# Performance work log

Hardware: AMD Instinct MI355X
Metric: run time of the kernel (lower is better)

The kernel has to match this reference:

```python
import jax, jax.numpy as jnp
import numpy as np
from jax import lax

B = 2          # graphs per batch
N_PER = 8192   # points per graph
K = 64         # max_num_neighbors in radius()
RATIO1, R1 = 0.5, 0.2
RATIO2, R2 = 0.25, 0.4


def _init(key, shape):
    return 0.1 * jax.random.normal(key, shape, jnp.float32)


def setup_inputs() -> dict:
    key = jax.random.key(0)
    ks = jax.random.split(key, 16)
    inp = {}
    inp["pos"] = jax.random.uniform(ks[0], (B * N_PER, 3), jnp.float32)
    inp["batch"] = jnp.repeat(jnp.arange(B, dtype=jnp.int32), N_PER)
    i = 1
    for name, dims in [("sa1", [(3, 64), (64, 64), (64, 128)]),
                       ("sa2", [(131, 128), (128, 128), (128, 256)])]:
        for j, (a, b) in enumerate(dims, 1):
            inp[f"{name}_W{j}"] = _init(ks[i], (a, b)); i += 1
            inp[f"{name}_b{j}"] = jnp.zeros((b,), jnp.float32)
    for name, (a, b) in [("lin1", (256, 256)), ("lin2", (256, 128)), ("lin3", (128, 1))]:
        inp[f"{name}_W"] = _init(ks[i], (a, b)); i += 1
        inp[f"{name}_b"] = jnp.zeros((b,), jnp.float32)
    return inp


def _fps(pts, S):
    # farthest point sampling; pts [n,3] -> idx [S] (deterministic start at 0)
    n = pts.shape[0]
    d0 = jnp.full((n,), jnp.inf, pts.dtype)
    def body(carry, _):
        d, last = carry
        d = jnp.minimum(d, jnp.sum((pts - pts[last]) ** 2, axis=-1))
        nxt = jnp.argmax(d).astype(jnp.int32)
        return (d, nxt), last
    _, idx = lax.scan(body, (d0, jnp.int32(0)), None, length=S)
    return idx


def _mlp(h, Ws, bs):
    h = jax.nn.relu(h @ Ws[0] + bs[0])
    h = jax.nn.relu(h @ Ws[1] + bs[1])
    return h @ Ws[2] + bs[2]


def _sa(x, pos, ratio, r, Ws, bs):
    # PointNet++ set abstraction: FPS -> radius neighbors (<=K) -> edge MLP -> max
    # pos [B,n,3]; x [B,n,C] or None
    n = pos.shape[1]
    S = int(n * ratio)
    idx = jax.vmap(lambda p: _fps(p, S))(pos)                       # [B,S]
    q = jnp.take_along_axis(pos, idx[..., None], axis=1)             # [B,S,3]
    d2 = jnp.sum((q[:, :, None, :] - pos[:, None, :, :]) ** 2, -1)   # [B,S,n]
    d2 = jnp.where(d2 <= r * r, d2, jnp.inf)
    negd, nbr = lax.top_k(-d2, K)                                    # [B,S,K]
    valid = jnp.isfinite(negd)                                       # in-radius mask
    gat = jax.vmap(lambda a, i: a[i])                                # per-graph gather
    rel = gat(pos, nbr) - q[:, :, None, :]                           # [B,S,K,3]
    feat = rel if x is None else jnp.concatenate([gat(x, nbr), rel], axis=-1)
    h = _mlp(feat, Ws, bs)                                           # [B,S,K,C]
    h = jnp.where(valid[..., None], h, -jnp.inf)
    return jnp.max(h, axis=2), q                                     # scatter-max aggr


def reference(pos, batch,
              sa1_W1, sa1_b1, sa1_W2, sa1_b2, sa1_W3, sa1_b3,
              sa2_W1, sa2_b1, sa2_W2, sa2_b2, sa2_W3, sa2_b3,
              lin1_W, lin1_b, lin2_W, lin2_b, lin3_W, lin3_b):
    p = pos.reshape(B, N_PER, 3)  # batch ids are sorted, equal-sized graphs
    x1, p1 = _sa(None, p, RATIO1, R1,
                 (sa1_W1, sa1_W2, sa1_W3), (sa1_b1, sa1_b2, sa1_b3))
    x2, _ = _sa(x1, p1, RATIO2, R2,
                (sa2_W1, sa2_W2, sa2_W3), (sa2_b1, sa2_b2, sa2_b3))
    h = jax.nn.relu(x2 @ lin1_W + lin1_b)
    h = jax.nn.relu(h @ lin2_W + lin2_b)
    h = jax.nn.sigmoid(h @ lin3_W + lin3_b)
    return h.reshape(-1, 1)  # [B * N_PER * RATIO1 * RATIO2, 1]
```

## Files before the change

### kernel.cpp

```cpp
#include <hip/hip_runtime.h>
#include <math.h>

#define NEG_INF (-__builtin_inff())
#define POS_INF (__builtin_inff())

__device__ __forceinline__ int imax_i(int a, int b) { return a > b ? a : b; }

template<int CTRL, int RMASK>
__device__ __forceinline__ int dpp_imax_step(int y) {
  const int t = __builtin_amdgcn_update_dpp(y, y, CTRL, RMASK, 0xf, false);
  return imax_i(y, t);
}

template<int N, int PPT, int S, int NT>
__global__ __launch_bounds__(NT) void fpsp_kernel(const float* __restrict__ pos,
                                                  float* __restrict__ q_out)
{
  constexpr int CELLS = 4096;
  constexpr int CPT = CELLS / NT;
  static_assert(N == NT * PPT, "chunking");
  static_assert(S <= CELLS, "winner list fits in hist");

  const int b = blockIdx.x;
  const int t = threadIdx.x;
  pos += (size_t)b * N * 3;
  q_out += (size_t)b * S * 3;

  __shared__ float sxyz[3 * N];
  __shared__ int sorder[N];
  __shared__ int hist[CELLS];
  __shared__ int scanbuf[NT];
  __shared__ unsigned long long slot[4];

  int* const swin = hist;

  for (int i = t; i < CELLS; i += NT) hist[i] = 0;
  if (t < 4) slot[t] = 0;
  __syncthreads();
  for (int i = t; i < N; i += NT) {
    const float x = pos[3*i+0], y = pos[3*i+1], z = pos[3*i+2];
    sxyz[3*i+0] = x; sxyz[3*i+1] = y; sxyz[3*i+2] = z;
    int cx = (int)(x * 16.f); cx = cx < 0 ? 0 : (cx > 15 ? 15 : cx);
    int cy = (int)(y * 16.f); cy = cy < 0 ? 0 : (cy > 15 ? 15 : cy);
    int cz = (int)(z * 16.f); cz = cz < 0 ? 0 : (cz > 15 ? 15 : cz);
    int m = 0;
#pragma unroll
    for (int k = 0; k < 4; ++k)
      m |= (((cx >> k) & 1) << (3*k+2)) | (((cy >> k) & 1) << (3*k+1)) | (((cz >> k) & 1) << (3*k));
    atomicAdd(&hist[m], 1);
  }
  __syncthreads();
  int loc[CPT]; int run = 0;
#pragma unroll
  for (int j = 0; j < CPT; ++j) { loc[j] = run; run += hist[t*CPT + j]; }
  scanbuf[t] = run;
  __syncthreads();
  for (int off = 1; off < NT; off <<= 1) {
    const int o = (t >= off) ? scanbuf[t - off] : 0;
    __syncthreads();
    scanbuf[t] += o;
    __syncthreads();
  }
  const int base = scanbuf[t] - run;
#pragma unroll
  for (int j = 0; j < CPT; ++j) hist[t*CPT + j] = base + loc[j];
  __syncthreads();
  for (int i = t; i < N; i += NT) {
    const float x = sxyz[3*i+0], y = sxyz[3*i+1], z = sxyz[3*i+2];
    int cx = (int)(x * 16.f); cx = cx < 0 ? 0 : (cx > 15 ? 15 : cx);
    int cy = (int)(y * 16.f); cy = cy < 0 ? 0 : (cy > 15 ? 15 : cy);
    int cz = (int)(z * 16.f); cz = cz < 0 ? 0 : (cz > 15 ? 15 : cz);
    int m = 0;
#pragma unroll
    for (int k = 0; k < 4; ++k)
      m |= (((cx >> k) & 1) << (3*k+2)) | (((cy >> k) & 1) << (3*k+1)) | (((cz >> k) & 1) << (3*k));
    const int sl = atomicAdd(&hist[m], 1);
    sorder[sl] = i;
  }
  __syncthreads();
  float px[PPT], py[PPT], pz[PPT], d[PPT];
  int og[PPT];
  float bxmin = POS_INF, bxmax = NEG_INF, bymin = POS_INF, bymax = NEG_INF,
        bzmin = POS_INF, bzmax = NEG_INF;
#pragma unroll
  for (int j = 0; j < PPT; ++j) {
    const int o = sorder[t*PPT + j];
    og[j] = o;
    const float x = sxyz[3*o+0], y = sxyz[3*o+1], z = sxyz[3*o+2];
    px[j] = x; py[j] = y; pz[j] = z;
    bxmin = fminf(bxmin, x); bxmax = fmaxf(bxmax, x);
    bymin = fminf(bymin, y); bymax = fmaxf(bymax, y);
    bzmin = fminf(bzmin, z); bzmax = fmaxf(bzmax, z);
    d[j] = POS_INF;
  }
  __syncthreads();

  const int lane = t & 63;
  float cval = POS_INF;
  int corig = 0x7fffffff;
  int wmvb = 0;
  int wwo = 0x7fffffff;
  int worig = 0;
  int p = 0;

  for (int it = 0; it < S; ++it) {
    if (t == 0) swin[it] = worig;
    const float lx = sxyz[3*worig+0], ly = sxyz[3*worig+1], lz = sxyz[3*worig+2];

    const float ddx = fmaxf(0.f, fmaxf(bxmin - lx, lx - bxmax));
    const float ddy = fmaxf(0.f, fmaxf(bymin - ly, ly - bymax));
    const float ddz = fmaxf(0.f, fmaxf(bzmin - lz, lz - bzmax));
    const float mind2 = ddx*ddx + ddy*ddy + ddz*ddz;
    const bool rec = !(mind2 * 0.99999f >= cval);

    if (rec) {
      float bv = -1.f; int bo = 0x7fffffff;
#pragma unroll
      for (int j = 0; j < PPT; ++j) {
        const float dx = __fsub_rn(px[j], lx);
        const float dy = __fsub_rn(py[j], ly);
        const float dz = __fsub_rn(pz[j], lz);
        const float nd = __fadd_rn(__fadd_rn(__fmul_rn(dx, dx), __fmul_rn(dy, dy)),
                                   __fmul_rn(dz, dz));
        const float dn = __builtin_fminf(d[j], nd);
        d[j] = dn;
        if (dn > bv || (dn == bv && og[j] < bo)) { bv = dn; bo = og[j]; }
      }
      cval = bv; corig = bo;
    }

    if (__ballot(rec) != 0ULL) {
      const int x = __float_as_int(cval);
      int y = x;
      y = dpp_imax_step<0x111, 0xf>(y);
      y = dpp_imax_step<0x112, 0xf>(y);
      y = dpp_imax_step<0x114, 0xf>(y);
      y = dpp_imax_step<0x118, 0xf>(y);
      y = dpp_imax_step<0x142, 0xa>(y);
      y = dpp_imax_step<0x143, 0xc>(y);
      wmvb = __builtin_amdgcn_readlane(y, 63);
      unsigned long long tie = __ballot(__float_as_int(cval) == wmvb);
      int wo = 0x7fffffff;
      while (tie) {
        const int l = __builtin_ctzll(tie);
        const int o = __builtin_amdgcn_readlane(corig, l);
        wo = wo < o ? wo : o;
        tie &= tie - 1;
      }
      wwo = wo;
    }

    if (lane == 0)
      atomicMax(&slot[p], ((unsigned long long)(unsigned)wmvb << 32) |
                          (unsigned)~(unsigned)wwo);
    if (t == 0) slot[(p + 1) & 3] = 0;
    __syncthreads();
    const unsigned long long wm = slot[p];
    worig = (int)(~(unsigned)(wm & 0xffffffffULL));
    p = (p + 1) & 3;
  }

  __syncthreads();
  for (int s = t; s < S; s += NT) {
    const int o = swin[s];
    q_out[3*s+0] = sxyz[3*o+0]; q_out[3*s+1] = sxyz[3*o+1]; q_out[3*s+2] = sxyz[3*o+2];
  }
}

struct Prod2S {
  unsigned long long slot[4];
  float sxyz[3 * 4096];
  int sorder[4096];
  int hist[4096];
  int scanbuf[1024];
};
struct Cons1S {
  unsigned long long keys[2048];
  float sW2[64 * 64];
  float sW3[64 * 128];
  float sW1[3 * 64];
  float sb1[64], sb2[64], sb3[128];
  float h1[64][65];
  float h2b[64][65];
  float featT[3][64];
  int snb[64];
  int s_cnt;
};
constexpr size_t SMC = sizeof(Prod2S) > sizeof(Cons1S) ? sizeof(Prod2S) : sizeof(Cons1S);

__global__ __launch_bounds__(1024)
void combo2_kernel(const float* __restrict__ pos,
                   const float* __restrict__ q1,
                   float* __restrict__ q2,
                   float* __restrict__ x1,
                   const float* __restrict__ W1, const float* __restrict__ b1,
                   const float* __restrict__ W2, const float* __restrict__ b2,
                   const float* __restrict__ W3, const float* __restrict__ b3)
{
  __shared__ __align__(16) char smraw[SMC];
  const int bid = blockIdx.x;
  const int t = threadIdx.x;

  if (bid < 2) {
    constexpr int N = 4096, PPT = 4, S = 1024, NT = 1024;
    constexpr int CELLS = 4096, CPT = CELLS / NT;
    Prod2S& P = *reinterpret_cast<Prod2S*>(smraw);
    const float* pb = q1 + (size_t)bid * N * 3;
    float* qb = q2 + (size_t)bid * S * 3;
    int* const swin = P.hist;

    for (int i = t; i < CELLS; i += NT) P.hist[i] = 0;
    if (t < 4) P.slot[t] = 0;
    __syncthreads();
    for (int i = t; i < N; i += NT) {
      const float x = pb[3*i+0], y = pb[3*i+1], z = pb[3*i+2];
      P.sxyz[3*i+0] = x; P.sxyz[3*i+1] = y; P.sxyz[3*i+2] = z;
      int cx = (int)(x * 16.f); cx = cx < 0 ? 0 : (cx > 15 ? 15 : cx);
      int cy = (int)(y * 16.f); cy = cy < 0 ? 0 : (cy > 15 ? 15 : cy);
      int cz = (int)(z * 16.f); cz = cz < 0 ? 0 : (cz > 15 ? 15 : cz);
      int m = 0;
#pragma unroll
      for (int k = 0; k < 4; ++k)
        m |= (((cx >> k) & 1) << (3*k+2)) | (((cy >> k) & 1) << (3*k+1)) | (((cz >> k) & 1) << (3*k));
      atomicAdd(&P.hist[m], 1);
    }
    __syncthreads();
    int loc[CPT]; int run = 0;
#pragma unroll
    for (int j = 0; j < CPT; ++j) { loc[j] = run; run += P.hist[t*CPT + j]; }
    P.scanbuf[t] = run;
    __syncthreads();
    for (int off = 1; off < NT; off <<= 1) {
      const int o = (t >= off) ? P.scanbuf[t - off] : 0;
      __syncthreads();
      P.scanbuf[t] += o;
      __syncthreads();
    }
    const int base = P.scanbuf[t] - run;
#pragma unroll
    for (int j = 0; j < CPT; ++j) P.hist[t*CPT + j] = base + loc[j];
    __syncthreads();
    for (int i = t; i < N; i += NT) {
      const float x = P.sxyz[3*i+0], y = P.sxyz[3*i+1], z = P.sxyz[3*i+2];
      int cx = (int)(x * 16.f); cx = cx < 0 ? 0 : (cx > 15 ? 15 : cx);
      int cy = (int)(y * 16.f); cy = cy < 0 ? 0 : (cy > 15 ? 15 : cy);
      int cz = (int)(z * 16.f); cz = cz < 0 ? 0 : (cz > 15 ? 15 : cz);
      int m = 0;
#pragma unroll
      for (int k = 0; k < 4; ++k)
        m |= (((cx >> k) & 1) << (3*k+2)) | (((cy >> k) & 1) << (3*k+1)) | (((cz >> k) & 1) << (3*k));
      const int sl = atomicAdd(&P.hist[m], 1);
      P.sorder[sl] = i;
    }
    __syncthreads();
    float px[PPT], py[PPT], pz[PPT], d[PPT];
    int og[PPT];
    float bxmin = POS_INF, bxmax = NEG_INF, bymin = POS_INF, bymax = NEG_INF,
          bzmin = POS_INF, bzmax = NEG_INF;
#pragma unroll
    for (int j = 0; j < PPT; ++j) {
      const int o = P.sorder[t*PPT + j];
      og[j] = o;
      const float x = P.sxyz[3*o+0], y = P.sxyz[3*o+1], z = P.sxyz[3*o+2];
      px[j] = x; py[j] = y; pz[j] = z;
      bxmin = fminf(bxmin, x); bxmax = fmaxf(bxmax, x);
      bymin = fminf(bymin, y); bymax = fmaxf(bymax, y);
      bzmin = fminf(bzmin, z); bzmax = fmaxf(bzmax, z);
      d[j] = POS_INF;
    }
    __syncthreads();

    const int lane = t & 63;
    float cval = POS_INF;
    int corig = 0x7fffffff;
    int wmvb = 0;
    int wwo = 0x7fffffff;
    int worig = 0;
    int p = 0;

    for (int it = 0; it < S; ++it) {
      if (t == 0) swin[it] = worig;
      const float lx = P.sxyz[3*worig+0], ly = P.sxyz[3*worig+1], lz = P.sxyz[3*worig+2];

      const float ddx = fmaxf(0.f, fmaxf(bxmin - lx, lx - bxmax));
      const float ddy = fmaxf(0.f, fmaxf(bymin - ly, ly - bymax));
      const float ddz = fmaxf(0.f, fmaxf(bzmin - lz, lz - bzmax));
      const float mind2 = ddx*ddx + ddy*ddy + ddz*ddz;
      const bool rec = !(mind2 * 0.99999f >= cval);

      if (rec) {
        float bv = -1.f; int bo = 0x7fffffff;
#pragma unroll
        for (int j = 0; j < PPT; ++j) {
          const float dx = __fsub_rn(px[j], lx);
          const float dy = __fsub_rn(py[j], ly);
          const float dz = __fsub_rn(pz[j], lz);
          const float nd = __fadd_rn(__fadd_rn(__fmul_rn(dx, dx), __fmul_rn(dy, dy)),
                                     __fmul_rn(dz, dz));
          const float dn = __builtin_fminf(d[j], nd);
          d[j] = dn;
          if (dn > bv || (dn == bv && og[j] < bo)) { bv = dn; bo = og[j]; }
        }
        cval = bv; corig = bo;
      }

      if (__ballot(rec) != 0ULL) {
        const int x = __float_as_int(cval);
        int y = x;
        y = dpp_imax_step<0x111, 0xf>(y);
        y = dpp_imax_step<0x112, 0xf>(y);
        y = dpp_imax_step<0x114, 0xf>(y);
        y = dpp_imax_step<0x118, 0xf>(y);
        y = dpp_imax_step<0x142, 0xa>(y);
        y = dpp_imax_step<0x143, 0xc>(y);
        wmvb = __builtin_amdgcn_readlane(y, 63);
        unsigned long long tie = __ballot(__float_as_int(cval) == wmvb);
        int wo = 0x7fffffff;
        while (tie) {
          const int l = __builtin_ctzll(tie);
          const int o = __builtin_amdgcn_readlane(corig, l);
          wo = wo < o ? wo : o;
          tie &= tie - 1;
        }
        wwo = wo;
      }

      if (lane == 0)
        atomicMax(&P.slot[p], ((unsigned long long)(unsigned)wmvb << 32) |
                              (unsigned)~(unsigned)wwo);
      if (t == 0) P.slot[(p + 1) & 3] = 0;
      __syncthreads();
      const unsigned long long wm = P.slot[p];
      worig = (int)(~(unsigned)(wm & 0xffffffffULL));
      p = (p + 1) & 3;
    }

    __syncthreads();
    for (int s = t; s < S; s += NT) {
      const int o = swin[s];
      qb[3*s+0] = P.sxyz[3*o+0]; qb[3*s+1] = P.sxyz[3*o+1]; qb[3*s+2] = P.sxyz[3*o+2];
    }
    return;
  }

  Cons1S& C = *reinterpret_cast<Cons1S*>(smraw);
  const float R1SQ = (float)(0.2 * 0.2);
  const int qi = bid - 2;
  const int g = qi >> 12;
  const float* cb = pos + (size_t)g * 8192 * 3;
  const float qx = q1[3*qi+0], qy = q1[3*qi+1], qz = q1[3*qi+2];

  for (int i = t; i < 192; i += 1024) C.sW1[i] = W1[i];
  if (t < 64) { C.sb1[t] = b1[t]; C.sb2[t] = b2[t]; }
  for (int i = t; i < 4096; i += 1024) C.sW2[i] = W2[i];
  for (int i = t; i < 8192; i += 1024) C.sW3[i] = W3[i];
  if (t < 128) C.sb3[t] = b3[t];
  if (t == 0) C.s_cnt = 0;
  __syncthreads();

  for (int i = t; i < 8192; i += 1024) {
    const float dx = __fsub_rn(cb[3*i+0], qx);
    const float dy = __fsub_rn(cb[3*i+1], qy);
    const float dz = __fsub_rn(cb[3*i+2], qz);
    const float d2 = __fadd_rn(__fadd_rn(__fmul_rn(dx, dx), __fmul_rn(dy, dy)),
                               __fmul_rn(dz, dz));
    if (d2 <= R1SQ) {
      const int pp = atomicAdd(&C.s_cnt, 1);
      if (pp < 2048)
        C.keys[pp] = ((unsigned long long)__float_as_uint(d2) << 32) | (unsigned)i;
    }
  }
  __syncthreads();
  const int M = min(C.s_cnt, 2048);
  const int cnt = min(M, 64);
  if (M > 64) {
    int P2 = 128; while (P2 < M) P2 <<= 1;
    for (int i = M + t; i < P2; i += 1024) C.keys[i] = ~0ULL;
    __syncthreads();
    for (int k = 2; k <= P2; k <<= 1) {
      for (int j = k >> 1; j > 0; j >>= 1) {
        for (int i = t; i < P2; i += 1024) {
          const int l = i ^ j;
          if (l > i) {
            const unsigned long long a = C.keys[i], c = C.keys[l];
            const bool up = ((i & k) == 0);
            if ((a > c) == up) { C.keys[i] = c; C.keys[l] = a; }
          }
        }
        __syncthreads();
      }
    }
  }
  if (t < 64) C.snb[t] = (t < cnt) ? (int)(C.keys[t] & 0xffffffffu) : 0;
  __syncthreads();

  const int e = t & 63, cg = t >> 6;
  if (t < 64) {
    float r0 = 0.f, r1 = 0.f, r2v = 0.f;
    if (t < cnt) {
      const int nb = C.snb[t];
      r0 = cb[3*nb+0] - qx;
      r1 = cb[3*nb+1] - qy;
      r2v = cb[3*nb+2] - qz;
    }
    C.featT[0][t] = r0; C.featT[1][t] = r1; C.featT[2][t] = r2v;
  }
  __syncthreads();
  {
    const int c0 = cg * 4;
    const float a0 = C.featT[0][e], a1 = C.featT[1][e], a2 = C.featT[2][e];
#pragma unroll
    for (int i = 0; i < 4; ++i) {
      float v = C.sb1[c0+i];
      v = fmaf(a0, C.sW1[0*64 + c0+i], v);
      v = fmaf(a1, C.sW1[1*64 + c0+i], v);
      v = fmaf(a2, C.sW1[2*64 + c0+i], v);
      C.h1[e][c0+i] = fmaxf(v, 0.f);
    }
  }
  __syncthreads();
  {
    const int c0 = cg * 4;
    float acc[4];
#pragma unroll
    for (int i = 0; i < 4; ++i) acc[i] = C.sb2[c0+i];
    for (int k = 0; k < 64; ++k) {
      const float a = C.h1[e][k];
      const float4 w = *reinterpret_cast<const float4*>(&C.sW2[k*64 + c0]);
      acc[0] = fmaf(a, w.x, acc[0]);
      acc[1] = fmaf(a, w.y, acc[1]);
      acc[2] = fmaf(a, w.z, acc[2]);
      acc[3] = fmaf(a, w.w, acc[3]);
    }
#pragma unroll
    for (int i = 0; i < 4; ++i) C.h2b[e][c0+i] = fmaxf(acc[i], 0.f);
  }
  __syncthreads();
  float acc3[8];
  const int c0h = cg * 8;
  {
#pragma unroll
    for (int i = 0; i < 8; ++i) acc3[i] = C.sb3[c0h+i];
    for (int k = 0; k < 64; ++k) {
      const float a = C.h2b[e][k];
      const float4* wp = reinterpret_cast<const float4*>(&C.sW3[k*128 + c0h]);
      const float4 w0 = wp[0], w1 = wp[1];
      acc3[0] = fmaf(a, w0.x, acc3[0]);
      acc3[1] = fmaf(a, w0.y, acc3[1]);
      acc3[2] = fmaf(a, w0.z, acc3[2]);
      acc3[3] = fmaf(a, w0.w, acc3[3]);
      acc3[4] = fmaf(a, w1.x, acc3[4]);
      acc3[5] = fmaf(a, w1.y, acc3[5]);
      acc3[6] = fmaf(a, w1.z, acc3[6]);
      acc3[7] = fmaf(a, w1.w, acc3[7]);
    }
  }
  __syncthreads();
  {
    const bool valid = (e < cnt);
#pragma unroll
    for (int i = 0; i < 8; ++i) {
      const float v = valid ? acc3[i] : NEG_INF;
      const int c = c0h + i;
      if (c < 64) C.h1[e][c] = v; else C.h2b[e][c-64] = v;
    }
  }
  __syncthreads();
  if (t < 128) {
    float m = NEG_INF;
    if (t < 64) {
      for (int ee = 0; ee < 64; ++ee) m = fmaxf(m, C.h1[ee][t]);
    } else {
      for (int ee = 0; ee < 64; ++ee) m = fmaxf(m, C.h2b[ee][t-64]);
    }
    x1[(size_t)qi*128 + t] = m;
  }
}

#define KNN_CAP 2048

__global__ __launch_bounds__(256) void knn_kernel(const float* __restrict__ cand,
                                                  const float* __restrict__ qpos,
                                                  int nq_per_graph, int n_cand, float r2,
                                                  int* __restrict__ nbr_out,
                                                  int* __restrict__ cnt_out)
{
  const int qi = blockIdx.x;
  const int t = threadIdx.x;
  const int b = qi / nq_per_graph;
  const float* cb = cand + (size_t)b * n_cand * 3;
  const float qx = qpos[3*qi+0], qy = qpos[3*qi+1], qz = qpos[3*qi+2];

  __shared__ unsigned long long keys[KNN_CAP];
  __shared__ int s_cnt;
  if (t == 0) s_cnt = 0;
  __syncthreads();

  for (int i = t; i < n_cand; i += 256) {
    const float dx = __fsub_rn(cb[3*i+0], qx);
    const float dy = __fsub_rn(cb[3*i+1], qy);
    const float dz = __fsub_rn(cb[3*i+2], qz);
    const float d2 = __fadd_rn(__fadd_rn(__fmul_rn(dx, dx), __fmul_rn(dy, dy)),
                               __fmul_rn(dz, dz));
    if (d2 <= r2) {
      const int p = atomicAdd(&s_cnt, 1);
      if (p < KNN_CAP) keys[p] = ((unsigned long long)__float_as_uint(d2) << 32) | (unsigned)i;
    }
  }
  __syncthreads();
  const int M = min(s_cnt, KNN_CAP);
  const int out_n = min(M, 64);
  if (M > 64) {
    int P = 128; while (P < M) P <<= 1;
    for (int i = M + t; i < P; i += 256) keys[i] = ~0ULL;
    __syncthreads();
    for (int k = 2; k <= P; k <<= 1) {
      for (int j = k >> 1; j > 0; j >>= 1) {
        for (int i = t; i < P; i += 256) {
          const int l = i ^ j;
          if (l > i) {
            const unsigned long long a = keys[i], c = keys[l];
            const bool up = ((i & k) == 0);
            if ((a > c) == up) { keys[i] = c; keys[l] = a; }
          }
        }
        __syncthreads();
      }
    }
  }
  if (t < 64) nbr_out[(size_t)qi*64 + t] = (t < out_n) ? (int)(keys[t] & 0xffffffffu) : -1;
  if (t == 0) cnt_out[qi] = out_n;
}

__global__ __launch_bounds__(256) void mlp2_kernel(const float* __restrict__ q1,
                                                   const float* __restrict__ x1,
                                                   const float* __restrict__ q2,
                                                   const int* __restrict__ nbr,
                                                   const int* __restrict__ cnt_,
                                                   const float* __restrict__ W1, const float* __restrict__ b1,
                                                   const float* __restrict__ W2, const float* __restrict__ b2,
                                                   const float* __restrict__ W3, const float* __restrict__ b3,
                                                   float* __restrict__ x2)
{
  const int qi = blockIdx.x;
  const int t = threadIdx.x;
  const int bg = qi >> 10;
  const float* cb = q1 + (size_t)bg * 4096 * 3;
  const float* xb = x1 + (size_t)bg * 4096 * 128;

  __shared__ float sW[131*128];
  __shared__ float sb[256];
  __shared__ float featT[131][64];
  __shared__ float hbuf[64][129];
  __shared__ int snb[64];

  const int cnt = cnt_[qi];
  const float qx = q2[3*qi+0], qy = q2[3*qi+1], qz = q2[3*qi+2];

  if (t < 64) {
    const int nb = (t < cnt) ? nbr[(size_t)qi*64 + t] : 0;
    snb[t] = nb;
    float r0 = 0.f, r1 = 0.f, r2v = 0.f;
    if (t < cnt) {
      r0 = cb[3*nb+0] - qx;
      r1 = cb[3*nb+1] - qy;
      r2v = cb[3*nb+2] - qz;
    }
    featT[128][t] = r0; featT[129][t] = r1; featT[130][t] = r2v;
  }
  for (int i = t; i < 131*128; i += 256) sW[i] = W1[i];
  if (t < 128) sb[t] = b1[t];
  __syncthreads();
  for (int idx = t; idx < 64*128; idx += 256) {
    const int e = idx >> 7, k = idx & 127;
    featT[k][e] = (e < cnt) ? xb[(size_t)snb[e]*128 + k] : 0.f;
  }
  __syncthreads();

  const int e = t & 63, cg = t >> 6, c0 = cg * 32;
  float acc[32];
  {
#pragma unroll
    for (int i = 0; i < 32; ++i) acc[i] = sb[c0+i];
    for (int k = 0; k < 131; ++k) {
      const float a = featT[k][e];
      const float4* wp = reinterpret_cast<const float4*>(&sW[k*128 + c0]);
#pragma unroll
      for (int i = 0; i < 8; ++i) {
        const float4 w = wp[i];
        acc[4*i+0] = fmaf(a, w.x, acc[4*i+0]);
        acc[4*i+1] = fmaf(a, w.y, acc[4*i+1]);
        acc[4*i+2] = fmaf(a, w.z, acc[4*i+2]);
        acc[4*i+3] = fmaf(a, w.w, acc[4*i+3]);
      }
    }
#pragma unroll
    for (int i = 0; i < 32; ++i) hbuf[e][c0+i] = fmaxf(acc[i], 0.f);
  }
  __syncthreads();
  for (int i = t; i < 128*128; i += 256) sW[i] = W2[i];
  if (t < 128) sb[t] = b2[t];
  __syncthreads();
  {
#pragma unroll
    for (int i = 0; i < 32; ++i) acc[i] = sb[c0+i];
    for (int k = 0; k < 128; ++k) {
      const float a = hbuf[e][k];
      const float4* wp = reinterpret_cast<const float4*>(&sW[k*128 + c0]);
#pragma unroll
      for (int i = 0; i < 8; ++i) {
        const float4 w = wp[i];
        acc[4*i+0] = fmaf(a, w.x, acc[4*i+0]);
        acc[4*i+1] = fmaf(a, w.y, acc[4*i+1]);
        acc[4*i+2] = fmaf(a, w.z, acc[4*i+2]);
        acc[4*i+3] = fmaf(a, w.w, acc[4*i+3]);
      }
    }
  }
  __syncthreads();
#pragma unroll
  for (int i = 0; i < 32; ++i) featT[c0+i][e] = fmaxf(acc[i], 0.f);
  __syncthreads();
  for (int hh = 0; hh < 2; ++hh) {
    for (int i = t; i < 128*128; i += 256) {
      const int k = i >> 7, c = i & 127;
      sW[i] = W3[k*256 + hh*128 + c];
    }
    if (t < 128) sb[t] = b3[hh*128 + t];
    __syncthreads();
#pragma unroll
    for (int i = 0; i < 32; ++i) acc[i] = sb[c0+i];
    for (int k = 0; k < 128; ++k) {
      const float a = featT[k][e];
      const float4* wp = reinterpret_cast<const float4*>(&sW[k*128 + c0]);
#pragma unroll
      for (int i = 0; i < 8; ++i) {
        const float4 w = wp[i];
        acc[4*i+0] = fmaf(a, w.x, acc[4*i+0]);
        acc[4*i+1] = fmaf(a, w.y, acc[4*i+1]);
        acc[4*i+2] = fmaf(a, w.z, acc[4*i+2]);
        acc[4*i+3] = fmaf(a, w.w, acc[4*i+3]);
      }
    }
    const bool valid = (e < cnt);
#pragma unroll
    for (int i = 0; i < 32; ++i) hbuf[e][c0+i] = valid ? acc[i] : NEG_INF;
    __syncthreads();
    if (t < 128) {
      float m = NEG_INF;
      for (int ee = 0; ee < 64; ++ee) m = fmaxf(m, hbuf[ee][t]);
      x2[(size_t)qi*256 + hh*128 + t] = m;
    }
    __syncthreads();
  }
}

__global__ __launch_bounds__(256) void head_kernel(const float* __restrict__ x2,
                                                   const float* __restrict__ W1, const float* __restrict__ b1,
                                                   const float* __restrict__ W2, const float* __restrict__ b2,
                                                   const float* __restrict__ W3, const float* __restrict__ b3,
                                                   float* __restrict__ out)
{
  const int pt = blockIdx.x;
  const int t = threadIdx.x;
  __shared__ float sx[256];
  __shared__ float sh1[256];
  __shared__ float sh2[128];
  __shared__ float red[128];

  sx[t] = x2[(size_t)pt*256 + t];
  __syncthreads();
  float a1 = b1[t];
  for (int k = 0; k < 256; ++k) a1 = fmaf(sx[k], W1[k*256 + t], a1);
  sh1[t] = fmaxf(a1, 0.f);
  __syncthreads();
  if (t < 128) {
    float a2 = b2[t];
    for (int k = 0; k < 256; ++k) a2 = fmaf(sh1[k], W2[k*128 + t], a2);
    sh2[t] = fmaxf(a2, 0.f);
  }
  __syncthreads();
  if (t < 128) red[t] = sh2[t] * W3[t];
  __syncthreads();
  for (int o = 64; o > 0; o >>= 1) {
    if (t < o) red[t] += red[t + o];
    __syncthreads();
  }
  if (t == 0) {
    const float v = red[0] + b3[0];
    out[pt] = 1.f / (1.f + expf(-v));
  }
}

extern "C" void kernel_launch(void* const* d_in, const int* in_sizes, int n_in,
                              void* d_out, int out_size, void* d_ws, size_t ws_size,
                              hipStream_t stream)
{
  (void)in_sizes; (void)n_in; (void)out_size; (void)ws_size;
  const float* pos  = (const float*)d_in[0];
  const float* s1W1 = (const float*)d_in[2];  const float* s1b1 = (const float*)d_in[3];
  const float* s1W2 = (const float*)d_in[4];  const float* s1b2 = (const float*)d_in[5];
  const float* s1W3 = (const float*)d_in[6];  const float* s1b3 = (const float*)d_in[7];
  const float* s2W1 = (const float*)d_in[8];  const float* s2b1 = (const float*)d_in[9];
  const float* s2W2 = (const float*)d_in[10]; const float* s2b2 = (const float*)d_in[11];
  const float* s2W3 = (const float*)d_in[12]; const float* s2b3 = (const float*)d_in[13];
  const float* l1W  = (const float*)d_in[14]; const float* l1b  = (const float*)d_in[15];
  const float* l2W  = (const float*)d_in[16]; const float* l2b  = (const float*)d_in[17];
  const float* l3W  = (const float*)d_in[18]; const float* l3b  = (const float*)d_in[19];
  float* out = (float*)d_out;

  char* w = (char*)d_ws;
  size_t off = 0;
  auto alloc = [&](size_t bytes) -> void* {
    void* p = w + off;
    off += (bytes + 255) & ~(size_t)255;
    return p;
  };
  float* q1   = (float*)alloc((size_t)2*4096*3*4);
  float* q2   = (float*)alloc((size_t)2*1024*3*4);
  float* x1   = (float*)alloc((size_t)8192*128*4);
  float* x2   = (float*)alloc((size_t)2048*256*4);
  int*   nbr2 = (int*)alloc((size_t)2048*64*4);
  int*   cnt2 = (int*)alloc((size_t)2048*4);

  const float R2SQ = (float)(0.4 * 0.4);

  fpsp_kernel<8192, 8, 4096, 1024><<<dim3(2), dim3(1024), 0, stream>>>(pos, q1);
  combo2_kernel<<<dim3(8194), dim3(1024), 0, stream>>>(pos, q1, q2, x1,
                                                       s1W1, s1b1, s1W2, s1b2, s1W3, s1b3);
  knn_kernel<<<dim3(2048), dim3(256), 0, stream>>>(q1, q2, 1024, 4096, R2SQ, nbr2, cnt2);
  mlp2_kernel<<<dim3(2048), dim3(256), 0, stream>>>(q1, x1, q2, nbr2, cnt2,
                                                    s2W1, s2b1, s2W2, s2b2, s2W3, s2b3, x2);
  head_kernel<<<dim3(2048), dim3(256), 0, stream>>>(x2, l1W, l1b, l2W, l2b, l3W, l3b, out);
}
```

Baseline: 4.794 ms.

## Fuse radius kNN, SA2 edge MLP and head MLP into one tail kernel

```diff
diff --git a/kernel.cpp b/kernel.cpp
--- a/kernel.cpp
+++ b/kernel.cpp
@@ -479,101 +479,98 @@
 
 #define KNN_CAP 2048
 
-__global__ __launch_bounds__(256) void knn_kernel(const float* __restrict__ cand,
-                                                  const float* __restrict__ qpos,
-                                                  int nq_per_graph, int n_cand, float r2,
-                                                  int* __restrict__ nbr_out,
-                                                  int* __restrict__ cnt_out)
+struct TailS {
+  union {
+    unsigned long long keys[KNN_CAP];
+    float sW[131*128];
+  } u;
+  float sb[256];
+  float featT[131][64];
+  float hbuf[64][129];
+  int snb[64];
+  int s_cnt;
+  float x2row[256];
+  float sh1[256];
+  float sh2[128];
+  float red[128];
+};
+
+__global__ __launch_bounds__(256)
+void tail_kernel(const float* __restrict__ q1,
+                 const float* __restrict__ x1,
+                 const float* __restrict__ q2,
+                 const float* __restrict__ W1, const float* __restrict__ b1,
+                 const float* __restrict__ W2, const float* __restrict__ b2,
+                 const float* __restrict__ W3, const float* __restrict__ b3,
+                 const float* __restrict__ hW1, const float* __restrict__ hb1,
+                 const float* __restrict__ hW2, const float* __restrict__ hb2,
+                 const float* __restrict__ hW3, const float* __restrict__ hb3,
+                 float* __restrict__ out)
 {
+  __shared__ __align__(16) TailS S;
   const int qi = blockIdx.x;
   const int t = threadIdx.x;
-  const int b = qi / nq_per_graph;
-  const float* cb = cand + (size_t)b * n_cand * 3;
-  const float qx = qpos[3*qi+0], qy = qpos[3*qi+1], qz = qpos[3*qi+2];
-
-  __shared__ unsigned long long keys[KNN_CAP];
-  __shared__ int s_cnt;
-  if (t == 0) s_cnt = 0;
-  __syncthreads();
-
-  for (int i = t; i < n_cand; i += 256) {
+  const int bg = qi >> 10;
+  const float* cb = q1 + (size_t)bg * 4096 * 3;
+  const float* xb = x1 + (size_t)bg * 4096 * 128;
+  const float R2SQ = (float)(0.4 * 0.4);
+
+  const float qx = q2[3*qi+0], qy = q2[3*qi+1], qz = q2[3*qi+2];
+
+  if (t == 0) S.s_cnt = 0;
+  __syncthreads();
+  for (int i = t; i < 4096; i += 256) {
     const float dx = __fsub_rn(cb[3*i+0], qx);
     const float dy = __fsub_rn(cb[3*i+1], qy);
     const float dz = __fsub_rn(cb[3*i+2], qz);
     const float d2 = __fadd_rn(__fadd_rn(__fmul_rn(dx, dx), __fmul_rn(dy, dy)),
                                __fmul_rn(dz, dz));
-    if (d2 <= r2) {
-      const int p = atomicAdd(&s_cnt, 1);
-      if (p < KNN_CAP) keys[p] = ((unsigned long long)__float_as_uint(d2) << 32) | (unsigned)i;
-    }
-  }
-  __syncthreads();
-  const int M = min(s_cnt, KNN_CAP);
-  const int out_n = min(M, 64);
+    if (d2 <= R2SQ) {
+      const int p = atomicAdd(&S.s_cnt, 1);
+      if (p < KNN_CAP)
+        S.u.keys[p] = ((unsigned long long)__float_as_uint(d2) << 32) | (unsigned)i;
+    }
+  }
+  __syncthreads();
+  const int M = min(S.s_cnt, KNN_CAP);
+  const int cnt = min(M, 64);
   if (M > 64) {
     int P = 128; while (P < M) P <<= 1;
-    for (int i = M + t; i < P; i += 256) keys[i] = ~0ULL;
+    for (int i = M + t; i < P; i += 256) S.u.keys[i] = ~0ULL;
     __syncthreads();
     for (int k = 2; k <= P; k <<= 1) {
       for (int j = k >> 1; j > 0; j >>= 1) {
         for (int i = t; i < P; i += 256) {
           const int l = i ^ j;
           if (l > i) {
-            const unsigned long long a = keys[i], c = keys[l];
+            const unsigned long long a = S.u.keys[i], c = S.u.keys[l];
             const bool up = ((i & k) == 0);
-            if ((a > c) == up) { keys[i] = c; keys[l] = a; }
+            if ((a > c) == up) { S.u.keys[i] = c; S.u.keys[l] = a; }
           }
         }
         __syncthreads();
       }
     }
   }
-  if (t < 64) nbr_out[(size_t)qi*64 + t] = (t < out_n) ? (int)(keys[t] & 0xffffffffu) : -1;
-  if (t == 0) cnt_out[qi] = out_n;
-}
-
-__global__ __launch_bounds__(256) void mlp2_kernel(const float* __restrict__ q1,
-                                                   const float* __restrict__ x1,
-                                                   const float* __restrict__ q2,
-                                                   const int* __restrict__ nbr,
-                                                   const int* __restrict__ cnt_,
-                                                   const float* __restrict__ W1, const float* __restrict__ b1,
-                                                   const float* __restrict__ W2, const float* __restrict__ b2,
-                                                   const float* __restrict__ W3, const float* __restrict__ b3,
-                                                   float* __restrict__ x2)
-{
-  const int qi = blockIdx.x;
-  const int t = threadIdx.x;
-  const int bg = qi >> 10;
-  const float* cb = q1 + (size_t)bg * 4096 * 3;
-  const float* xb = x1 + (size_t)bg * 4096 * 128;
-
-  __shared__ float sW[131*128];
-  __shared__ float sb[256];
-  __shared__ float featT[131][64];
-  __shared__ float hbuf[64][129];
-  __shared__ int snb[64];
-
-  const int cnt = cnt_[qi];
-  const float qx = q2[3*qi+0], qy = q2[3*qi+1], qz = q2[3*qi+2];
+  if (t < 64) S.snb[t] = (t < cnt) ? (int)(S.u.keys[t] & 0xffffffffu) : 0;
+  __syncthreads();
 
   if (t < 64) {
-    const int nb = (t < cnt) ? nbr[(size_t)qi*64 + t] : 0;
-    snb[t] = nb;
+    const int nb = S.snb[t];
     float r0 = 0.f, r1 = 0.f, r2v = 0.f;
     if (t < cnt) {
       r0 = cb[3*nb+0] - qx;
       r1 = cb[3*nb+1] - qy;
       r2v = cb[3*nb+2] - qz;
     }
-    featT[128][t] = r0; featT[129][t] = r1; featT[130][t] = r2v;
-  }
-  for (int i = t; i < 131*128; i += 256) sW[i] = W1[i];
-  if (t < 128) sb[t] = b1[t];
+    S.featT[128][t] = r0; S.featT[129][t] = r1; S.featT[130][t] = r2v;
+  }
+  for (int i = t; i < 131*128; i += 256) S.u.sW[i] = W1[i];
+  if (t < 128) S.sb[t] = b1[t];
   __syncthreads();
   for (int idx = t; idx < 64*128; idx += 256) {
     const int e = idx >> 7, k = idx & 127;
-    featT[k][e] = (e < cnt) ? xb[(size_t)snb[e]*128 + k] : 0.f;
+    S.featT[k][e] = (e < cnt) ? xb[(size_t)S.snb[e]*128 + k] : 0.f;
   }
   __syncthreads();
 
@@ -581,10 +578,10 @@
   float acc[32];
   {
 #pragma unroll
-    for (int i = 0; i < 32; ++i) acc[i] = sb[c0+i];
+    for (int i = 0; i < 32; ++i) acc[i] = S.sb[c0+i];
     for (int k = 0; k < 131; ++k) {
-      const float a = featT[k][e];
-      const float4* wp = reinterpret_cast<const float4*>(&sW[k*128 + c0]);
+      const float a = S.featT[k][e];
+      const float4* wp = reinterpret_cast<const float4*>(&S.u.sW[k*128 + c0]);
 #pragma unroll
       for (int i = 0; i < 8; ++i) {
         const float4 w = wp[i];
@@ -595,18 +592,18 @@
       }
     }
 #pragma unroll
-    for (int i = 0; i < 32; ++i) hbuf[e][c0+i] = fmaxf(acc[i], 0.f);
-  }
-  __syncthreads();
-  for (int i = t; i < 128*128; i += 256) sW[i] = W2[i];
-  if (t < 128) sb[t] = b2[t];
+    for (int i = 0; i < 32; ++i) S.hbuf[e][c0+i] = fmaxf(acc[i], 0.f);
+  }
+  __syncthreads();
+  for (int i = t; i < 128*128; i += 256) S.u.sW[i] = W2[i];
+  if (t < 128) S.sb[t] = b2[t];
   __syncthreads();
   {
 #pragma unroll
-    for (int i = 0; i < 32; ++i) acc[i] = sb[c0+i];
+    for (int i = 0; i < 32; ++i) acc[i] = S.sb[c0+i];
     for (int k = 0; k < 128; ++k) {
-      const float a = hbuf[e][k];
-      const float4* wp = reinterpret_cast<const float4*>(&sW[k*128 + c0]);
+      const float a = S.hbuf[e][k];
+      const float4* wp = reinterpret_cast<const float4*>(&S.u.sW[k*128 + c0]);
 #pragma unroll
       for (int i = 0; i < 8; ++i) {
         const float4 w = wp[i];
@@ -619,20 +616,20 @@
   }
   __syncthreads();
 #pragma unroll
-  for (int i = 0; i < 32; ++i) featT[c0+i][e] = fmaxf(acc[i], 0.f);
+  for (int i = 0; i < 32; ++i) S.featT[c0+i][e] = fmaxf(acc[i], 0.f);
   __syncthreads();
   for (int hh = 0; hh < 2; ++hh) {
     for (int i = t; i < 128*128; i += 256) {
       const int k = i >> 7, c = i & 127;
-      sW[i] = W3[k*256 + hh*128 + c];
-    }
-    if (t < 128) sb[t] = b3[hh*128 + t];
-    __syncthreads();
-#pragma unroll
-    for (int i = 0; i < 32; ++i) acc[i] = sb[c0+i];
+      S.u.sW[i] = W3[k*256 + hh*128 + c];
+    }
+    if (t < 128) S.sb[t] = b3[hh*128 + t];
+    __syncthreads();
+#pragma unroll
+    for (int i = 0; i < 32; ++i) acc[i] = S.sb[c0+i];
     for (int k = 0; k < 128; ++k) {
-      const float a = featT[k][e];
-      const float4* wp = reinterpret_cast<const float4*>(&sW[k*128 + c0]);
+      const float a = S.featT[k][e];
+      const float4* wp = reinterpret_cast<const float4*>(&S.u.sW[k*128 + c0]);
 #pragma unroll
       for (int i = 0; i < 8; ++i) {
         const float4 w = wp[i];
@@ -644,51 +641,35 @@
     }
     const bool valid = (e < cnt);
 #pragma unroll
-    for (int i = 0; i < 32; ++i) hbuf[e][c0+i] = valid ? acc[i] : NEG_INF;
+    for (int i = 0; i < 32; ++i) S.hbuf[e][c0+i] = valid ? acc[i] : NEG_INF;
     __syncthreads();
     if (t < 128) {
       float m = NEG_INF;
-      for (int ee = 0; ee < 64; ++ee) m = fmaxf(m, hbuf[ee][t]);
-      x2[(size_t)qi*256 + hh*128 + t] = m;
-    }
-    __syncthreads();
-  }
-}
-
-__global__ __launch_bounds__(256) void head_kernel(const float* __restrict__ x2,
-                                                   const float* __restrict__ W1, const float* __restrict__ b1,
-                                                   const float* __restrict__ W2, const float* __restrict__ b2,
-                                                   const float* __restrict__ W3, const float* __restrict__ b3,
-                                                   float* __restrict__ out)
-{
-  const int pt = blockIdx.x;
-  const int t = threadIdx.x;
-  __shared__ float sx[256];
-  __shared__ float sh1[256];
-  __shared__ float sh2[128];
-  __shared__ float red[128];
-
-  sx[t] = x2[(size_t)pt*256 + t];
-  __syncthreads();
-  float a1 = b1[t];
-  for (int k = 0; k < 256; ++k) a1 = fmaf(sx[k], W1[k*256 + t], a1);
-  sh1[t] = fmaxf(a1, 0.f);
+      for (int ee = 0; ee < 64; ++ee) m = fmaxf(m, S.hbuf[ee][t]);
+      S.x2row[hh*128 + t] = m;
+    }
+    __syncthreads();
+  }
+
+  float a1 = hb1[t];
+  for (int k = 0; k < 256; ++k) a1 = fmaf(S.x2row[k], hW1[k*256 + t], a1);
+  S.sh1[t] = fmaxf(a1, 0.f);
   __syncthreads();
   if (t < 128) {
-    float a2 = b2[t];
-    for (int k = 0; k < 256; ++k) a2 = fmaf(sh1[k], W2[k*128 + t], a2);
-    sh2[t] = fmaxf(a2, 0.f);
-  }
-  __syncthreads();
-  if (t < 128) red[t] = sh2[t] * W3[t];
+    float a2 = hb2[t];
+    for (int k = 0; k < 256; ++k) a2 = fmaf(S.sh1[k], hW2[k*128 + t], a2);
+    S.sh2[t] = fmaxf(a2, 0.f);
+  }
+  __syncthreads();
+  if (t < 128) S.red[t] = S.sh2[t] * hW3[t];
   __syncthreads();
   for (int o = 64; o > 0; o >>= 1) {
-    if (t < o) red[t] += red[t + o];
+    if (t < o) S.red[t] += S.red[t + o];
     __syncthreads();
   }
   if (t == 0) {
-    const float v = red[0] + b3[0];
-    out[pt] = 1.f / (1.f + expf(-v));
+    const float v = S.red[0] + hb3[0];
+    out[qi] = 1.f / (1.f + expf(-v));
   }
 }
 
@@ -716,20 +697,14 @@
     off += (bytes + 255) & ~(size_t)255;
     return p;
   };
-  float* q1   = (float*)alloc((size_t)2*4096*3*4);
-  float* q2   = (float*)alloc((size_t)2*1024*3*4);
-  float* x1   = (float*)alloc((size_t)8192*128*4);
-  float* x2   = (float*)alloc((size_t)2048*256*4);
-  int*   nbr2 = (int*)alloc((size_t)2048*64*4);
-  int*   cnt2 = (int*)alloc((size_t)2048*4);
-
-  const float R2SQ = (float)(0.4 * 0.4);
+  float* q1 = (float*)alloc((size_t)2*4096*3*4);
+  float* q2 = (float*)alloc((size_t)2*1024*3*4);
+  float* x1 = (float*)alloc((size_t)8192*128*4);
 
   fpsp_kernel<8192, 8, 4096, 1024><<<dim3(2), dim3(1024), 0, stream>>>(pos, q1);
   combo2_kernel<<<dim3(8194), dim3(1024), 0, stream>>>(pos, q1, q2, x1,
                                                        s1W1, s1b1, s1W2, s1b2, s1W3, s1b3);
-  knn_kernel<<<dim3(2048), dim3(256), 0, stream>>>(q1, q2, 1024, 4096, R2SQ, nbr2, cnt2);
-  mlp2_kernel<<<dim3(2048), dim3(256), 0, stream>>>(q1, x1, q2, nbr2, cnt2,
-                                                    s2W1, s2b1, s2W2, s2b2, s2W3, s2b3, x2);
-  head_kernel<<<dim3(2048), dim3(256), 0, stream>>>(x2, l1W, l1b, l2W, l2b, l3W, l3b, out);
+  tail_kernel<<<dim3(2048), dim3(256), 0, stream>>>(q1, x1, q2,
+                                                    s2W1, s2b1, s2W2, s2b2, s2W3, s2b3,
+                                                    l1W, l1b, l2W, l2b, l3W, l3b, out);
 }
```

Result: slower. 5.019 ms (+4.7%).
